# Performance work log

Hardware: AMD Instinct MI355X
Metric: run time of the kernel (lower is better)

Reference implementation:

```python
import jax, jax.numpy as jnp
import numpy as np

B, C_IN, C_OUT, H, W = 4, 64, 64, 64, 64
D = 2 * C_OUT  # projected channel dim = 128


def conv1x1(x, w, b):
    # x: [B,Cin,H,W], w: [Cout,Cin], b: [Cout]
    return jnp.einsum('bchw,oc->bohw', x, w) + b[None, :, None, None]


def setup_inputs() -> dict:
    key = jax.random.key(0)
    ks = jax.random.split(key, 10)
    s_q = 1.0 / np.sqrt(C_IN)
    s_kv = 1.0 / np.sqrt(2 * C_IN)
    s_o = 1.0 / np.sqrt(D)
    return {
        'x_upper': jax.random.normal(ks[0], (B, C_IN, H, W), jnp.float32),
        'x_lower': jax.random.normal(ks[1], (B, 2 * C_IN, H, W), jnp.float32),
        'wq': jax.random.uniform(ks[2], (D, C_IN), jnp.float32, -s_q, s_q),
        'bq': jax.random.uniform(ks[3], (D,), jnp.float32, -s_q, s_q),
        'wk': jax.random.uniform(ks[4], (D, 2 * C_IN), jnp.float32, -s_kv, s_kv),
        'bk': jax.random.uniform(ks[5], (D,), jnp.float32, -s_kv, s_kv),
        'wv': jax.random.uniform(ks[6], (D, 2 * C_IN), jnp.float32, -s_kv, s_kv),
        'bv': jax.random.uniform(ks[7], (D,), jnp.float32, -s_kv, s_kv),
        'wo': jax.random.uniform(ks[8], (D, D), jnp.float32, -s_o, s_o),
        'bo': jax.random.uniform(ks[9], (D,), jnp.float32, -s_o, s_o),
    }


def reference(x_upper, x_lower, wq, bq, wk, bk, wv, bv, wo, bo):
    q = conv1x1(x_upper, wq, bq)   # [B,D,H,W]
    k = conv1x1(x_lower, wk, bk)   # [B,D,H,W]
    v = conv1x1(x_lower, wv, bv)   # [B,D,H,W]
    b, d = q.shape[0], q.shape[1]
    # NOTE: the torch code uses .view (raw reshape), NOT a transpose --
    # faithful translation is a plain reshape of the contiguous NCHW tensor.
    qf = q.reshape(b, -1, d)       # [B, N, D], N = H*W
    kf = k.reshape(b, -1, d)
    vf = v.reshape(b, -1, d)
    scores = jnp.einsum('bnd,bmd->bnm', qf, kf) / (d ** 0.5)  # [B,N,N]
    attn = jax.nn.softmax(scores, axis=-1)
    of = jnp.einsum('bnm,bmd->bnd', attn, vf)  # [B,N,D]
    out = of.reshape(v.shape)                  # [B,D,H,W]
    out = conv1x1(out, wo, bo) + x_lower
    return out
```

## Files before the change

kernel.cpp:

```cpp
#include <hip/hip_runtime.h>
#include <math.h>

#define BB 4
#define CIN 64
#define CL 128
#define DD 128
#define HW 4096
#define NN 4096
#define TP 132
#define YP 136

typedef __attribute__((ext_vector_type(8))) __bf16 bf16x8;
typedef __attribute__((ext_vector_type(16))) float f32x16;

__device__ __forceinline__ unsigned short f2bf(float f) {
    unsigned u = __builtin_bit_cast(unsigned, f);
    u += 0x7fffu + ((u >> 16) & 1u);
    return (unsigned short)(u >> 16);
}
__device__ __forceinline__ unsigned pack2(float lo, float hi) {
    return (unsigned)f2bf(lo) | ((unsigned)f2bf(hi) << 16);
}
__device__ __forceinline__ float bf2f(unsigned s) {
    return __builtin_bit_cast(float, s << 16);
}
__device__ __forceinline__ unsigned pack_trunc(float lo, float hi) {
    return __builtin_amdgcn_perm(__builtin_bit_cast(unsigned, hi),
                                 __builtin_bit_cast(unsigned, lo), 0x07060302u);
}
__device__ __forceinline__ float exp2_fast(float x) {
#if __has_builtin(__builtin_amdgcn_exp2f)
    return __builtin_amdgcn_exp2f(x);
#else
    return __expf(x * 0.6931471805599453f);
#endif
}
__device__ __forceinline__ void async_copy16(const unsigned short* g,
                                             unsigned short* l) {
    __builtin_amdgcn_global_load_lds(
        (const __attribute__((address_space(1))) void*)g,
        (__attribute__((address_space(3))) void*)l, 16, 0, 0);
}

__device__ __forceinline__ void split8(const float xv[8], bf16x8* hi, bf16x8* lo) {
    union { unsigned u[4]; bf16x8 v; } H, L;
#pragma unroll
    for (int i = 0; i < 4; ++i) {
        float x0 = xv[2 * i], x1 = xv[2 * i + 1];
        H.u[i] = pack_trunc(x0, x1);
        float h0 = __builtin_bit_cast(float,
                     __builtin_bit_cast(unsigned, x0) & 0xffff0000u);
        float h1 = __builtin_bit_cast(float,
                     __builtin_bit_cast(unsigned, x1) & 0xffff0000u);
        L.u[i] = pack_trunc(x0 - h0, x1 - h1);
    }
    *hi = H.v; *lo = L.v;
}

__global__ __launch_bounds__(512) void proj_qkv_mfma(
    const float* __restrict__ xq, const float* __restrict__ wq,
    const float* __restrict__ bq, unsigned short* __restrict__ qout,
    const float* __restrict__ xl,
    const float* __restrict__ wk, const float* __restrict__ bk,
    const float* __restrict__ wv, const float* __restrict__ bv,
    unsigned short* __restrict__ kout, unsigned short* __restrict__ vout,
    float oscale)
{
    __shared__ __align__(16) char smem[135168];
    float* xsf = (float*)smem;
    unsigned short* ytk = (unsigned short*)(smem + 65536);
    unsigned short* ytv = (unsigned short*)(smem + 100352);

    const int tid = threadIdx.x;
    const int w = tid >> 6;
    const int lane = tid & 63;
    const int half = lane >> 5;
    const int l5 = lane & 31;

    if (blockIdx.x < 128) {
        const int b = blockIdx.x >> 5;
        const int tile = blockIdx.x & 31;
        const int px0 = tile * 128;
        const int g = w >> 2;
        const int ms = w & 3;

        {
            const float* src = xl + (size_t)b * CL * HW + px0
                             + (size_t)(lane >> 5) * HW + (lane & 31) * 4;
#pragma unroll
            for (int k = 0; k < 8; ++k) {
                int c = w * 8 + k;
                async_copy16((const unsigned short*)(src + (size_t)(2 * c) * HW),
                             (unsigned short*)(smem + c * 1024));
            }
        }

        const float* wsrc = g ? wv : wk;
        const float* bsrc = g ? bv : bk;
        bf16x8 Ah[8];
        {
            const float* wr = wsrc + (size_t)(ms * 32 + l5) * CL + half * 8;
#pragma unroll
            for (int ks = 0; ks < 8; ++ks) {
                float tmp[8];
                *(float4*)&tmp[0] = *(const float4*)(wr + ks * 16);
                *(float4*)&tmp[4] = *(const float4*)(wr + ks * 16 + 4);
                union { unsigned u[4]; bf16x8 v; } H;
#pragma unroll
                for (int i = 0; i < 4; ++i)
                    H.u[i] = pack2(tmp[2 * i], tmp[2 * i + 1]);
                Ah[ks] = H.v;
            }
        }
        float biasr[16];
#pragma unroll
        for (int r = 0; r < 16; ++r)
            biasr[r] = bsrc[ms * 32 + (r & 3) + 8 * (r >> 2) + 4 * half];

        f32x16 acc[4];
#pragma unroll
        for (int ns = 0; ns < 4; ++ns)
#pragma unroll
            for (int r = 0; r < 16; ++r) acc[ns][r] = biasr[r];

        asm volatile("s_waitcnt vmcnt(0)" ::: "memory");
        __builtin_amdgcn_s_barrier();
        asm volatile("" ::: "memory");

#pragma unroll
        for (int ns = 0; ns < 4; ++ns) {
            int pxl = ns * 32 + l5;
#pragma unroll
            for (int ks = 0; ks < 8; ++ks) {
                int kb_ = ks * 16 + half * 8;
                union { unsigned u[4]; bf16x8 v; } B;
#pragma unroll
                for (int j = 0; j < 4; ++j)
                    B.u[j] = pack_trunc(xsf[(kb_ + 2 * j) * 128 + pxl],
                                        xsf[(kb_ + 2 * j + 1) * 128 + pxl]);
                acc[ns] = __builtin_amdgcn_mfma_f32_32x32x16_bf16(Ah[ks], B.v, acc[ns], 0, 0, 0);
            }
        }

        unsigned short* yt = g ? ytv : ytk;
#pragma unroll
        for (int ns = 0; ns < 4; ++ns) {
            int pxl = ns * 32 + l5;
#pragma unroll
            for (int r = 0; r < 16; ++r) {
                int o = ms * 32 + (r & 3) + 8 * (r >> 2) + 4 * half;
                yt[o * YP + pxl] = f2bf(acc[ns][r]);
            }
        }
        __syncthreads();

        unsigned short* kbase = kout + (size_t)b * NN * DD;
        unsigned short* vbase = vout + (size_t)b * 128 * HW + px0;
        const int tm = tile & 15;
#pragma unroll
        for (int i = 0; i < 4; ++i) {
            int e = tid + i * 512;
            int o = e >> 4, q = e & 15;
            uint4 kq4 = *(const uint4*)(ytk + o * YP + q * 8);
            *(uint4*)(kbase + (size_t)(o * 32 + tile) * 128 + ((q ^ tm) * 8)) = kq4;
            uint4 vq4 = *(const uint4*)(ytv + o * YP + q * 8);
            *(uint4*)(vbase + (size_t)o * HW + q * 8) = vq4;
        }
    } else {
        const int qb_ = blockIdx.x - 128;
        const int b = qb_ >> 5;
        const int tile = qb_ & 31;
        const int px0 = tile * 128;
        const int ms = w & 3;
        const int nsg = w >> 2;

        {
            const float* src = xq + (size_t)b * CIN * HW + px0
                             + (size_t)(lane >> 5) * HW + (lane & 31) * 4;
#pragma unroll
            for (int k = 0; k < 4; ++k) {
                int c = w * 4 + k;
                async_copy16((const unsigned short*)(src + (size_t)(2 * c) * HW),
                             (unsigned short*)(smem + c * 1024));
            }
        }

        bf16x8 Ah[4];
        {
            const float* wr = wq + (size_t)(ms * 32 + l5) * CIN + half * 8;
#pragma unroll
            for (int ks = 0; ks < 4; ++ks) {
                float tmp[8];
                *(float4*)&tmp[0] = *(const float4*)(wr + ks * 16);
                *(float4*)&tmp[4] = *(const float4*)(wr + ks * 16 + 4);
                union { unsigned u[4]; bf16x8 v; } H;
#pragma unroll
                for (int i = 0; i < 4; ++i)
                    H.u[i] = pack2(tmp[2 * i], tmp[2 * i + 1]);
                Ah[ks] = H.v;
            }
        }
        float biasr[16];
#pragma unroll
        for (int r = 0; r < 16; ++r)
            biasr[r] = bq[ms * 32 + (r & 3) + 8 * (r >> 2) + 4 * half];

        f32x16 acc[2];
#pragma unroll
        for (int i = 0; i < 2; ++i)
#pragma unroll
            for (int r = 0; r < 16; ++r) acc[i][r] = biasr[r];

        asm volatile("s_waitcnt vmcnt(0)" ::: "memory");
        __builtin_amdgcn_s_barrier();
        asm volatile("" ::: "memory");

#pragma unroll
        for (int i = 0; i < 2; ++i) {
            int pxl = (nsg * 2 + i) * 32 + l5;
#pragma unroll
            for (int ks = 0; ks < 4; ++ks) {
                int kb_ = ks * 16 + half * 8;
                union { unsigned u[4]; bf16x8 v; } B;
#pragma unroll
                for (int j = 0; j < 4; ++j)
                    B.u[j] = pack_trunc(xsf[(kb_ + 2 * j) * 128 + pxl],
                                        xsf[(kb_ + 2 * j + 1) * 128 + pxl]);
                acc[i] = __builtin_amdgcn_mfma_f32_32x32x16_bf16(Ah[ks], B.v, acc[i], 0, 0, 0);
            }
        }

#pragma unroll
        for (int i = 0; i < 2; ++i) {
            int pxl = (nsg * 2 + i) * 32 + l5;
#pragma unroll
            for (int r = 0; r < 16; ++r) {
                int o = ms * 32 + (r & 3) + 8 * (r >> 2) + 4 * half;
                ytk[o * YP + pxl] = f2bf(acc[i][r] * oscale);
            }
        }
        __syncthreads();

        unsigned short* qbase = qout + (size_t)b * 128 * HW + px0;
#pragma unroll
        for (int i = 0; i < 4; ++i) {
            int e = tid + i * 512;
            int o = e >> 4, q = e & 15;
            uint4 qq4 = *(const uint4*)(ytk + o * YP + q * 8);
            *(uint4*)(qbase + (size_t)o * HW + q * 8) = qq4;
        }
    }
}

__global__ __launch_bounds__(512) void proj_o_mfma(
    const unsigned short* __restrict__ x, const float* __restrict__ w,
    const float* __restrict__ bias, const float* __restrict__ resid,
    float* __restrict__ out)
{
    __shared__ __align__(16) unsigned short xs16[128 * 64];

    const int tid = threadIdx.x;
    const int w_ = tid >> 6;
    const int lane = tid & 63;
    const int half = lane >> 5;
    const int l5 = lane & 31;
    const int b = blockIdx.x >> 6;
    const int tile = blockIdx.x & 63;
    const int px0 = tile * 64;
    const int ms = w_ & 3;
    const int pxh = w_ >> 2;

    {
        const unsigned short* src = x + (size_t)b * DD * HW + px0
                                  + (size_t)(lane >> 3) * HW + (lane & 7) * 8;
#pragma unroll
        for (int k = 0; k < 2; ++k) {
            int c = w_ * 2 + k;
            async_copy16(src + (size_t)(8 * c) * HW, xs16 + c * 512);
        }
    }

    bf16x8 Ah[8], Al[8];
    {
        const float* wr = w + (size_t)(ms * 32 + l5) * DD + half * 8;
#pragma unroll
        for (int ks = 0; ks < 8; ++ks) {
            float tmp[8];
            *(float4*)&tmp[0] = *(const float4*)(wr + ks * 16);
            *(float4*)&tmp[4] = *(const float4*)(wr + ks * 16 + 4);
            split8(tmp, &Ah[ks], &Al[ks]);
        }
    }
    f32x16 acc;
#pragma unroll
    for (int r = 0; r < 16; ++r)
        acc[r] = bias[ms * 32 + (r & 3) + 8 * (r >> 2) + 4 * half];

    asm volatile("s_waitcnt vmcnt(0)" ::: "memory");
    __builtin_amdgcn_s_barrier();
    asm volatile("" ::: "memory");

    {
        int pxl = pxh * 32 + l5;
#pragma unroll
        for (int ks = 0; ks < 8; ++ks) {
            int kb_ = ks * 16 + half * 8;
            union { unsigned u[4]; bf16x8 v; } B;
#pragma unroll
            for (int p = 0; p < 4; ++p) {
                unsigned e0 = xs16[(kb_ + 2 * p) * 64 + pxl];
                unsigned e1 = xs16[(kb_ + 2 * p + 1) * 64 + pxl];
                B.u[p] = e0 | (e1 << 16);
            }
            acc = __builtin_amdgcn_mfma_f32_32x32x16_bf16(Ah[ks], B.v, acc, 0, 0, 0);
            acc = __builtin_amdgcn_mfma_f32_32x32x16_bf16(Al[ks], B.v, acc, 0, 0, 0);
        }
    }

    {
        int px = px0 + pxh * 32 + l5;
#pragma unroll
        for (int r = 0; r < 16; ++r) {
            int o = ms * 32 + (r & 3) + 8 * (r >> 2) + 4 * half;
            size_t a = ((size_t)b * 128 + o) * HW + px;
            out[a] = acc[r] + resid[a];
        }
    }
}

__global__ __launch_bounds__(256) void transpose_v(
    const unsigned short* __restrict__ vf, unsigned short* __restrict__ vt)
{
    __shared__ unsigned short tld[16 * TP];
    int tid = threadIdx.x;
    int b = blockIdx.x >> 8;
    int n0 = (blockIdx.x & 255) * 16;
    const unsigned short* src = vf + (size_t)b * NN * DD + (size_t)n0 * DD;
    {
        int n = tid >> 4, x = tid & 15;
        union { uint4 q; unsigned long long u[2]; } t;
        t.q = *(const uint4*)(src + (size_t)n * DD + x * 8);
        unsigned short* d = &tld[n * TP + x * 8];
        *(unsigned long long*)(d) = t.u[0];
        *(unsigned long long*)(d + 4) = t.u[1];
    }
    __syncthreads();
    unsigned short* dst = vt + (size_t)b * NN * DD + (size_t)(n0 >> 7) * 16384;
    int xb_ = (n0 & 127) >> 3;
    {
        int g = tid & 1, d = tid >> 1;
        union { uint4 q; unsigned short s[8]; } t;
#pragma unroll
        for (int j = 0; j < 8; ++j) t.s[j] = tld[(g * 8 + j) * TP + d];
        int xs = (xb_ + g) ^ (d & 15);
        *(uint4*)(dst + (size_t)d * 128 + xs * 8) = t.q;
    }
}

__global__ __launch_bounds__(512) void attn_mfma(
    const unsigned short* __restrict__ qf, const unsigned short* __restrict__ kfs,
    const unsigned short* __restrict__ vts, unsigned short* __restrict__ of)
{
    __shared__ __align__(16) char smem[133632];

    const int tid = threadIdx.x;
    const int lane = tid & 63;
    const int w = tid >> 6;
    const int kq = w & 3;
    const int rh = w >> 2;
    const int half = lane >> 5;
    const int l5 = lane & 31;
    const int b = blockIdx.x >> 6;
    const int rb0 = (blockIdx.x & 63) * 64;
    const int rw0 = rb0 + rh * 32;
    const int cw = kq * 32;

    const unsigned short* qb = qf + (size_t)b * NN * DD;
    const unsigned short* kb = kfs + (size_t)b * NN * DD;
    const unsigned short* vb = vts + (size_t)b * NN * DD;

    bf16x8 qfrag[8];
    {
        const unsigned short* qrow = qb + (size_t)(rw0 + l5) * DD + half * 8;
#pragma unroll
        for (int kk = 0; kk < 8; ++kk)
            qfrag[kk] = *(const bf16x8*)(qrow + kk * 16);
    }

    f32x16 O[4] = {};
    float lacc = 0.f;

    auto stage = [&](int t, int buf) {
        const unsigned short* kt = kb + (size_t)t * 16384;
        const unsigned short* vt_ = vb + (size_t)t * 16384;
        unsigned short* kl = (unsigned short*)(smem + buf * 65536);
        unsigned short* vl = kl + 16384;
#pragma unroll
        for (int j = 0; j < 4; ++j) {
            int c = (w * 4 + j) * 512;
            async_copy16(kt + c + lane * 8, kl + c);
            async_copy16(vt_ + c + lane * 8, vl + c);
        }
    };

    stage(0, 0);
    stage(1, 1);

    const int NT = NN / 128;
    for (int t = 0; t < NT; ++t) {
        const int cur = t & 1;
        if (t < NT - 1) asm volatile("s_waitcnt vmcnt(8)" ::: "memory");
        else            asm volatile("s_waitcnt vmcnt(0)" ::: "memory");
        __builtin_amdgcn_s_barrier();
        asm volatile("" ::: "memory");

        const unsigned short* kl = (const unsigned short*)(smem + cur * 65536);
        const unsigned short* vl = kl + 16384;

        f32x16 S = {};
        __builtin_amdgcn_s_setprio(1);
#pragma unroll
        for (int kk = 0; kk < 8; ++kk) {
            bf16x8 kfr = *(const bf16x8*)
                &kl[(cw + l5) * 128 + (((kk * 2 + half) ^ (l5 & 15)) * 8)];
            S = __builtin_amdgcn_mfma_f32_32x32x16_bf16(kfr, qfrag[kk], S, 0, 0, 0);
        }
        __builtin_amdgcn_s_setprio(0);

        float p[16];
#pragma unroll
        for (int r = 0; r < 16; ++r) p[r] = exp2_fast(S[r]);
        {
            float t0 = (p[0] + p[1]) + (p[2] + p[3]);
            float t1 = (p[4] + p[5]) + (p[6] + p[7]);
            float t2 = (p[8] + p[9]) + (p[10] + p[11]);
            float t3 = (p[12] + p[13]) + (p[14] + p[15]);
            lacc += (t0 + t1) + (t2 + t3);
        }

#pragma unroll
        for (int kc = 0; kc < 2; ++kc) {
            unsigned PA0 = pack_trunc(p[8 * kc + 0], p[8 * kc + 1]);
            unsigned PA1 = pack_trunc(p[8 * kc + 2], p[8 * kc + 3]);
            unsigned PB0 = pack_trunc(p[8 * kc + 4], p[8 * kc + 5]);
            unsigned PB1 = pack_trunc(p[8 * kc + 6], p[8 * kc + 7]);
            unsigned snd0 = half ? PA0 : PB0;
            unsigned snd1 = half ? PA1 : PB1;
            unsigned rcv0 = (unsigned)__shfl_xor((int)snd0, 32, 64);
            unsigned rcv1 = (unsigned)__shfl_xor((int)snd1, 32, 64);
            union { unsigned u[4]; bf16x8 v; } pf;
            pf.u[0] = half ? rcv0 : PA0;
            pf.u[1] = half ? rcv1 : PA1;
            pf.u[2] = half ? PB0 : rcv0;
            pf.u[3] = half ? PB1 : rcv1;
            __builtin_amdgcn_s_setprio(1);
#pragma unroll
            for (int ds = 0; ds < 4; ++ds) {
                bf16x8 vfr = *(const bf16x8*)
                    &vl[(ds * 32 + l5) * 128 +
                        (((kq * 4 + kc * 2 + half) ^ (l5 & 15)) * 8)];
                O[ds] = __builtin_amdgcn_mfma_f32_32x32x16_bf16(vfr, pf.v, O[ds], 0, 0, 0);
            }
            __builtin_amdgcn_s_setprio(0);
        }

        asm volatile("s_waitcnt lgkmcnt(0)" ::: "memory");
        __builtin_amdgcn_s_barrier();
        asm volatile("" ::: "memory");
        if (t + 2 < NT) stage(t + 2, cur);
    }

    lacc += __shfl_xor(lacc, 32, 64);

    float (*red_o)[64][129] = (float (*)[64][129])smem;
    float* red_l = (float*)(smem + 132096);
    if (half == 0) red_l[kq * 64 + rh * 32 + l5] = lacc;
#pragma unroll
    for (int ds = 0; ds < 4; ++ds)
#pragma unroll
        for (int r = 0; r < 16; ++r) {
            int d = ds * 32 + (r & 3) + 8 * (r >> 2) + 4 * half;
            red_o[kq][rh * 32 + l5][d] = O[ds][r];
        }
    __syncthreads();

    {
        int q = tid >> 3;
        int dg = tid & 7;
        float l = red_l[q] + red_l[64 + q] + red_l[128 + q] + red_l[192 + q];
        float inv = 1.f / l;
        unsigned outw[8];
#pragma unroll
        for (int i = 0; i < 8; ++i) {
            int d0 = dg * 16 + i * 2;
            float s0 = red_o[0][q][d0] + red_o[1][q][d0] +
                       red_o[2][q][d0] + red_o[3][q][d0];
            float s1 = red_o[0][q][d0 + 1] + red_o[1][q][d0 + 1] +
                       red_o[2][q][d0 + 1] + red_o[3][q][d0 + 1];
            outw[i] = pack2(s0 * inv, s1 * inv);
        }
        unsigned short* ob = of + (size_t)b * NN * DD + (size_t)(rb0 + q) * DD + dg * 16;
        *(uint4*)(ob) = *(uint4*)&outw[0];
        *(uint4*)(ob + 8) = *(uint4*)&outw[4];
    }
}

extern "C" void kernel_launch(void* const* d_in, const int* in_sizes, int n_in,
                              void* d_out, int out_size, void* d_ws, size_t ws_size,
                              hipStream_t stream) {
    const float* x_upper = (const float*)d_in[0];
    const float* x_lower = (const float*)d_in[1];
    const float* wq = (const float*)d_in[2];
    const float* bq = (const float*)d_in[3];
    const float* wk = (const float*)d_in[4];
    const float* bk = (const float*)d_in[5];
    const float* wv = (const float*)d_in[6];
    const float* bv = (const float*)d_in[7];
    const float* wo = (const float*)d_in[8];
    const float* bo = (const float*)d_in[9];
    float* out = (float*)d_out;

    const size_t ELT = (size_t)BB * NN * DD;
    unsigned short* qf  = (unsigned short*)d_ws;
    unsigned short* kfs = qf + ELT;
    unsigned short* vts = kfs + ELT;
    unsigned short* vfn = vts + ELT;
    unsigned short* ofb = vfn + ELT;

    const float qscale = (float)(0.08838834764831845 * 1.4426950408889634);

    proj_qkv_mfma<<<256, 512, 0, stream>>>(x_upper, wq, bq, qf,
                                           x_lower, wk, bk, wv, bv,
                                           kfs, vfn, qscale);
    transpose_v<<<1024, 256, 0, stream>>>(vfn, vts);
    attn_mfma<<<BB * 64, 512, 0, stream>>>(qf, kfs, vts, ofb);
    proj_o_mfma<<<256, 512, 0, stream>>>(ofb, wo, bo, x_lower, out);
}
```

Before: 147.4 us.

## Load K fragments directly from global into registers, stage only V in LDS

The projection kernel now writes K in plain NCHW layout (same as V before transposition) instead of a swizzled tiled layout. The attention kernel no longer stages K through shared memory; each wave loads its K fragments for the next tile straight into registers, prefetched one iteration ahead, and only V goes through the double-buffered LDS pipeline. This halves LDS traffic and the async copies per tile, but each of the four row-half wave groups now reloads the same K rows from global/L2 and adds 32 VGPRs for the prefetch buffer.

```diff
diff --git a/kernel.cpp b/kernel.cpp
--- a/kernel.cpp
+++ b/kernel.cpp
@@ -154,15 +154,14 @@
         }
         __syncthreads();
 
-        unsigned short* kbase = kout + (size_t)b * NN * DD;
+        unsigned short* kbase = kout + (size_t)b * 128 * HW + px0;
         unsigned short* vbase = vout + (size_t)b * 128 * HW + px0;
-        const int tm = tile & 15;
 #pragma unroll
         for (int i = 0; i < 4; ++i) {
             int e = tid + i * 512;
             int o = e >> 4, q = e & 15;
             uint4 kq4 = *(const uint4*)(ytk + o * YP + q * 8);
-            *(uint4*)(kbase + (size_t)(o * 32 + tile) * 128 + ((q ^ tm) * 8)) = kq4;
+            *(uint4*)(kbase + (size_t)o * HW + q * 8) = kq4;
             uint4 vq4 = *(const uint4*)(ytv + o * YP + q * 8);
             *(uint4*)(vbase + (size_t)o * HW + q * 8) = vq4;
         }
@@ -358,7 +357,7 @@
 }
 
 __global__ __launch_bounds__(512) void attn_mfma(
-    const unsigned short* __restrict__ qf, const unsigned short* __restrict__ kfs,
+    const unsigned short* __restrict__ qf, const unsigned short* __restrict__ kfn,
     const unsigned short* __restrict__ vts, unsigned short* __restrict__ of)
 {
     __shared__ __align__(16) char smem[133632];
@@ -376,7 +375,7 @@
     const int cw = kq * 32;
 
     const unsigned short* qb = qf + (size_t)b * NN * DD;
-    const unsigned short* kb = kfs + (size_t)b * NN * DD;
+    const unsigned short* kb = kfn + (size_t)b * NN * DD;
     const unsigned short* vb = vts + (size_t)b * NN * DD;
 
     bf16x8 qfrag[8];
@@ -387,45 +386,49 @@
             qfrag[kk] = *(const bf16x8*)(qrow + kk * 16);
     }
 
+    bf16x8 kpre[8];
+    auto kload = [&](int t) {
+        const unsigned short* kr = kb + ((size_t)t * 128 + cw + l5) * DD + half * 8;
+#pragma unroll
+        for (int kk = 0; kk < 8; ++kk)
+            kpre[kk] = *(const bf16x8*)(kr + kk * 16);
+    };
+
     f32x16 O[4] = {};
     float lacc = 0.f;
 
-    auto stage = [&](int t, int buf) {
-        const unsigned short* kt = kb + (size_t)t * 16384;
+    auto stageV = [&](int t, int buf) {
         const unsigned short* vt_ = vb + (size_t)t * 16384;
-        unsigned short* kl = (unsigned short*)(smem + buf * 65536);
-        unsigned short* vl = kl + 16384;
+        unsigned short* vl = (unsigned short*)(smem + buf * 32768);
 #pragma unroll
         for (int j = 0; j < 4; ++j) {
             int c = (w * 4 + j) * 512;
-            async_copy16(kt + c + lane * 8, kl + c);
             async_copy16(vt_ + c + lane * 8, vl + c);
         }
     };
 
-    stage(0, 0);
-    stage(1, 1);
+    kload(0);
+    stageV(0, 0);
+    stageV(1, 1);
 
     const int NT = NN / 128;
     for (int t = 0; t < NT; ++t) {
         const int cur = t & 1;
-        if (t < NT - 1) asm volatile("s_waitcnt vmcnt(8)" ::: "memory");
+        if (t < NT - 1) asm volatile("s_waitcnt vmcnt(4)" ::: "memory");
         else            asm volatile("s_waitcnt vmcnt(0)" ::: "memory");
         __builtin_amdgcn_s_barrier();
         asm volatile("" ::: "memory");
 
-        const unsigned short* kl = (const unsigned short*)(smem + cur * 65536);
-        const unsigned short* vl = kl + 16384;
+        const unsigned short* vl = (const unsigned short*)(smem + cur * 32768);
 
         f32x16 S = {};
         __builtin_amdgcn_s_setprio(1);
 #pragma unroll
-        for (int kk = 0; kk < 8; ++kk) {
-            bf16x8 kfr = *(const bf16x8*)
-                &kl[(cw + l5) * 128 + (((kk * 2 + half) ^ (l5 & 15)) * 8)];
-            S = __builtin_amdgcn_mfma_f32_32x32x16_bf16(kfr, qfrag[kk], S, 0, 0, 0);
-        }
+        for (int kk = 0; kk < 8; ++kk)
+            S = __builtin_amdgcn_mfma_f32_32x32x16_bf16(kpre[kk], qfrag[kk], S, 0, 0, 0);
         __builtin_amdgcn_s_setprio(0);
+
+        if (t + 1 < NT) kload(t + 1);
 
         float p[16];
 #pragma unroll
@@ -467,7 +470,7 @@
         asm volatile("s_waitcnt lgkmcnt(0)" ::: "memory");
         __builtin_amdgcn_s_barrier();
         asm volatile("" ::: "memory");
-        if (t + 2 < NT) stage(t + 2, cur);
+        if (t + 2 < NT) stageV(t + 2, cur);
     }
 
     lacc += __shfl_xor(lacc, 32, 64);
@@ -522,8 +525,8 @@
 
     const size_t ELT = (size_t)BB * NN * DD;
     unsigned short* qf  = (unsigned short*)d_ws;
-    unsigned short* kfs = qf + ELT;
-    unsigned short* vts = kfs + ELT;
+    unsigned short* kfn = qf + ELT;
+    unsigned short* vts = kfn + ELT;
     unsigned short* vfn = vts + ELT;
     unsigned short* ofb = vfn + ELT;
 
@@ -531,8 +534,8 @@
 
     proj_qkv_mfma<<<256, 512, 0, stream>>>(x_upper, wq, bq, qf,
                                            x_lower, wk, bk, wv, bv,
-                                           kfs, vfn, qscale);
+                                           kfn, vfn, qscale);
     transpose_v<<<1024, 256, 0, stream>>>(vfn, vts);
-    attn_mfma<<<BB * 64, 512, 0, stream>>>(qf, kfs, vts, ofb);
+    attn_mfma<<<BB * 64, 512, 0, stream>>>(qf, kfn, vts, ofb);
     proj_o_mfma<<<256, 512, 0, stream>>>(ofb, wo, bo, x_lower, out);
 }
```

Result: slower. 178.4 us (+21.0%).
